# Kernel tuning notes

Measured on AMD Instinct MI355X. Metric: run time of the kernel, lower is better.

The kernel has to match this reference:

```python
import jax, jax.numpy as jnp
import numpy as np
import itertools

D_FEAT = 8      # feature dim per point
N_NBR = 16     # kNN neighbors (self.N)
ORDERS = (2, 3)
BIG = 99999999.0


def _to_select(N, order):
    # rows: [0] + each (order-1)-combination of {1..N-1}, first N-1 rows
    rows = [[0] + list(c) for c in itertools.combinations(range(1, N), order - 1)][:N - 1]
    return np.asarray(rows, dtype=np.int32)  # (N-1, order)


def setup_inputs() -> dict:
    key = jax.random.key(0)
    ks = jax.random.split(key, 18)
    B, NP, DM, DO, NM, PNM = 4, 4096, 16, 8, 64, 64
    r = lambda k, s: jax.random.normal(k, s, dtype=jnp.float32)
    return {
        "x": r(ks[0], (B, NP * D_FEAT)),
        "z": r(ks[1], (B, PNM)),
        "Wm2": r(ks[2], (2, DM)) * 0.5, "bm2": r(ks[3], (DM,)) * 0.1,
        "Wm3": r(ks[4], (3, DM)) * 0.5, "bm3": r(ks[5], (DM,)) * 0.1,
        "Wv2": r(ks[6], (2, DM)) * 0.5, "bv2": r(ks[7], (DM,)) * 0.1,
        "Wv3": r(ks[8], (3, DM)) * 0.5, "bv3": r(ks[9], (DM,)) * 0.1,
        "Wmx": r(ks[10], (2 * DM, DO)) * 0.1, "bmx": r(ks[11], (DO,)) * 0.1,
        "Wvx": r(ks[12], (2 * DM, NM)) * 0.1, "bvx": r(ks[13], (NM,)) * 0.1,
        "Wmz": r(ks[14], (PNM, DO)) * 0.1, "bmz": r(ks[15], (DO,)) * 0.1,
        "Wvz": r(ks[16], (PNM, NM)) * 0.1, "bvz": r(ks[17], (NM,)) * 0.1,
    }


def _forward(x, z, Wm2, bm2, Wm3, bm3, Wv2, bv2, Wv3, bv3,
             Wmx, bmx, Wvx, bvx, Wmz, bmz, Wvz, bvz):
    B = x.shape[0]
    NP = x.shape[1] // D_FEAT
    N = N_NBR
    x3 = x.reshape(B, NP, D_FEAT)

    # pairwise euclidean distances via gram trick (avoids B*NP*NP*D intermediate)
    n2 = jnp.sum(x3 * x3, axis=-1)                                   # (B, NP)
    d2 = n2[:, :, None] + n2[:, None, :] - 2.0 * jnp.einsum('bid,bjd->bij', x3, x3)
    dist = jnp.sqrt(jnp.maximum(d2, 0.0))                            # (B, NP, NP)
    dist = jnp.where(dist == 0.0, BIG, dist)                         # mask exact-zero distances
    diag = jnp.arange(NP)
    dist = dist.at[:, diag, diag].set(BIG)                           # self-distance (exactly 0 in torch)

    # N smallest, sorted ascending
    _, idx = jax.lax.top_k(-dist, N)                                 # idx: (B, NP, N)

    def order_feats(Wf, bf, order):
        ts = jnp.asarray(_to_select(N, order))                       # (N-1, order)
        sel = idx[:, :, ts]                                          # (B, NP, N-1, o)
        g = jax.vmap(lambda xb, sb: xb[sb])(x3, sel)                 # (B, NP, N-1, o, D)
        # Linear(order -> d_Mfeat) applied per feature-dim o-tuple, relu, mean over feature dims
        y = jax.nn.relu(jnp.einsum('bnrod,ok->bnrdk', g, Wf) + bf)   # (B, NP, N-1, D, K)
        return y.mean(axis=3).reshape(B, NP * (N - 1), -1)           # (B, NP*(N-1), K)

    moments = jnp.concatenate([order_feats(Wm2, bm2, 2), order_feats(Wm3, bm3, 3)], axis=-1)
    v_moments = jnp.concatenate([order_feats(Wv2, bv2, 2), order_feats(Wv3, bv3, 3)], axis=-1)

    d_out = Wmx.shape[1]
    x_new = jax.nn.relu(moments @ Wmx + bmx + (z @ Wmz + bmz)[:, None, :])
    x_new = x_new.reshape(B, NP, N - 1, d_out).mean(axis=2).reshape(B, NP * d_out)

    z_new = jax.nn.relu(v_moments @ Wvx + bvx + (z @ Wvz + bvz)[:, None, :]).mean(axis=1)
    return x_new, z_new


def reference(x, z, Wm2, bm2, Wm3, bm3, Wv2, bv2, Wv3, bv3,
              Wmx, bmx, Wvx, bvx, Wmz, bmz, Wvz, bvz):
    return _forward(x, z, Wm2, bm2, Wm3, bm3, Wv2, bv2, Wv3, bv3,
                    Wmx, bmx, Wvx, bvx, Wmz, bmz, Wvz, bvz)
```

## Files before the change

### kernel.cpp

```cpp
#include <hip/hip_runtime.h>
#include <hip/hip_bf16.h>

#define BIGF 99999999.0f
#define NPP 4096
#define BB 4
#define NQ 4


__device__ __forceinline__ float rl(float v, int l) {
    return __int_as_float(__builtin_amdgcn_readlane(__float_as_int(v), l));
}

template <typename T>
__device__ __forceinline__ T bitonic_sort64(T v, int lane) {
    #pragma unroll
    for (int k = 2; k <= 64; k <<= 1) {
        #pragma unroll
        for (int j = k >> 1; j > 0; j >>= 1) {
            T p = __shfl_xor(v, j);
            bool up  = ((lane & k) == 0);
            bool low = ((lane & j) == 0);
            T mn = (v < p) ? v : p;
            T mx = (v < p) ? p : v;
            v = (up == low) ? mn : mx;
        }
    }
    return v;
}

__device__ __forceinline__ unsigned d2key(const float* qf, float n2i,
                                          const float4& a, const float4& c,
                                          float n2j, int j, int q) {
    float dot = 0.f;
    dot = fmaf(qf[0], a.x, dot); dot = fmaf(qf[1], a.y, dot);
    dot = fmaf(qf[2], a.z, dot); dot = fmaf(qf[3], a.w, dot);
    dot = fmaf(qf[4], c.x, dot); dot = fmaf(qf[5], c.y, dot);
    dot = fmaf(qf[6], c.z, dot); dot = fmaf(qf[7], c.w, dot);
    float d2 = fmaf(-2.0f, dot, n2i + n2j);
    return (d2 <= 0.0f || j == q) ? __float_as_uint(BIGF) : __float_as_uint(d2);
}


__global__ __launch_bounds__(256) void n2_kernel(const float* __restrict__ x,
                                                 float* __restrict__ n2tab,
                                                 float* __restrict__ zout) {
    int i = blockIdx.x * 256 + threadIdx.x;
    if (blockIdx.x == 0) zout[threadIdx.x] = 0.f;
    const float4* p = (const float4*)(x + (long)i * 8);
    float4 a = p[0], c = p[1];
    float s = 0.f;
    s = fmaf(a.x, a.x, s); s = fmaf(a.y, a.y, s);
    s = fmaf(a.z, a.z, s); s = fmaf(a.w, a.w, s);
    s = fmaf(c.x, c.x, s); s = fmaf(c.y, c.y, s);
    s = fmaf(c.z, c.z, s); s = fmaf(c.w, c.w, s);
    n2tab[i] = s;
}


__global__ void zz_kernel(const float* __restrict__ z,
                          const float* __restrict__ Wmz, const float* __restrict__ bmz,
                          const float* __restrict__ Wvz, const float* __restrict__ bvz,
                          float* __restrict__ zzm, float* __restrict__ zzv) {
    int b = blockIdx.x, l = threadIdx.x;
    float sv = 0.f;
    for (int p = 0; p < 64; ++p) sv = fmaf(z[b * 64 + p], Wvz[p * 64 + l], sv);
    zzv[b * 64 + l] = sv + bvz[l];
    if (l < 8) {
        float sm = 0.f;
        for (int p = 0; p < 64; ++p) sm = fmaf(z[b * 64 + p], Wmz[p * 8 + l], sm);
        zzm[b * 8 + l] = sm + bmz[l];
    }
}


__global__ __launch_bounds__(256) void knn_kernel(const float* __restrict__ x,
                                                  const float* __restrict__ n2tab,
                                                  int* __restrict__ idx_out) {
    __shared__ unsigned long long cand[4][NQ][64];

    int lane = threadIdx.x & 63;
    int wid  = threadIdx.x >> 6;
    int gw   = blockIdx.x * 4 + wid;
    int q0   = gw * NQ;
    int b    = q0 >> 12;
    int qloc = q0 & 4095;
    const float* xb = x + (long)b * NPP * 8;
    const float* nb = n2tab + b * NPP;

    float qf[NQ][8];
    float n2i[NQ];
    #pragma unroll
    for (int q = 0; q < NQ; ++q) {
        #pragma unroll
        for (int f = 0; f < 8; ++f) qf[q][f] = xb[(qloc + q) * 8 + f];
        n2i[q] = nb[qloc + q];
    }

    unsigned minb[NQ];
    #pragma unroll
    for (int q = 0; q < NQ; ++q) minb[q] = 0xFFFFFFFFu;

    #pragma unroll 4
    for (int t = 0; t < 64; ++t) {
        int j = t * 64 + lane;
        const float4* pj = (const float4*)(xb + j * 8);
        float4 a = pj[0], c = pj[1];
        float n2j = nb[j];
        #pragma unroll
        for (int q = 0; q < NQ; ++q) {
            unsigned kb = d2key(qf[q], n2i[q], a, c, n2j, j, qloc + q);
            minb[q] = (kb < minb[q]) ? kb : minb[q];
        }
    }

    unsigned T[NQ];
    #pragma unroll
    for (int q = 0; q < NQ; ++q) {
        unsigned v = bitonic_sort64(minb[q], lane);
        T[q] = (unsigned)__shfl((int)v, 15);
    }

    int cnt[NQ];
    #pragma unroll
    for (int q = 0; q < NQ; ++q) cnt[q] = 0;

    for (int t = 0; t < 64; ++t) {
        int j = t * 64 + lane;
        const float4* pj = (const float4*)(xb + j * 8);
        float4 a = pj[0], c = pj[1];
        float n2j = nb[j];
        #pragma unroll
        for (int q = 0; q < NQ; ++q) {
            unsigned kb = d2key(qf[q], n2i[q], a, c, n2j, j, qloc + q);
            bool pred = (kb <= T[q]);
            unsigned long long m = __ballot(pred);
            if (m) {
                int ofs = cnt[q] + __popcll(m & ((1ull << lane) - 1ull));
                if (pred && ofs < 64) {
                    cand[wid][q][ofs] = ((unsigned long long)kb << 32) | (unsigned)j;
                }
                cnt[q] += __popcll(m);
            }
        }
    }

    #pragma unroll 1
    for (int q = 0; q < NQ; ++q) {
        int c = cnt[q] < 64 ? cnt[q] : 64;
        unsigned long long key = (lane < c) ? cand[wid][q][lane] : ~0ull;
        key = bitonic_sort64(key, lane);
        if (lane < 16) {
            idx_out[(long)(q0 + q) * 16 + lane] = (int)(key & 0xFFFFFFFFull);
        }
    }
}


__global__ __launch_bounds__(256) void feat_kernel(
    const float* __restrict__ x, const int* __restrict__ idxw,
    const float* __restrict__ Wm2, const float* __restrict__ bm2,
    const float* __restrict__ Wm3, const float* __restrict__ bm3,
    const float* __restrict__ Wv2, const float* __restrict__ bv2,
    const float* __restrict__ Wv3, const float* __restrict__ bv3,
    const float* __restrict__ Wmx, const float* __restrict__ bmx,
    const float* __restrict__ Wvx, const float* __restrict__ bvx,
    const float* __restrict__ zzm, const float* __restrict__ zzv,
    float* __restrict__ xout, float* __restrict__ zout)
{
    int lane = threadIdx.x & 63;
    int wid  = threadIdx.x >> 6;
    int pn   = blockIdx.x * 4 + wid;
    int b    = pn >> 12;
    const float* xb = x + b * NPP * 8;

    __shared__ float xg_s[4][16][8];
    __shared__ float mm_s[4][15][36];
    __shared__ float wmx_s[32][8];
    __shared__ float bzm_s[8];
    __shared__ float zpart[4][64];

    if (threadIdx.x < 256) {
        wmx_s[threadIdx.x >> 3][threadIdx.x & 7] = Wmx[threadIdx.x];
    }
    if (threadIdx.x < 8) bzm_s[threadIdx.x] = bmx[threadIdx.x] + zzm[b * 8 + threadIdx.x];

    int k = lane & 15;
    float w20 = Wm2[k], w21 = Wm2[16 + k], bb2 = bm2[k];
    float w30 = Wm3[k], w31 = Wm3[16 + k], w32 = Wm3[32 + k], bb3 = bm3[k];
    float u20 = Wv2[k], u21 = Wv2[16 + k], cc2 = bv2[k];
    float u30 = Wv3[k], u31 = Wv3[16 + k], u32 = Wv3[32 + k], cc3 = bv3[k];
    float wvx[32];
    #pragma unroll
    for (int c = 0; c < 32; ++c) wvx[c] = Wvx[c * 64 + lane];
    float bz3 = bvx[lane] + zzv[b * 64 + lane];

    if (lane < 16) {
        int myid = idxw[(long)pn * 16 + lane];
        const float4* ps = (const float4*)(xb + (long)myid * 8);
        float4 a = ps[0], c4 = ps[1];
        *((float4*)&xg_s[wid][lane][0]) = a;
        *((float4*)&xg_s[wid][lane][4]) = c4;
    }
    __syncthreads();

    float g0[8];
    #pragma unroll
    for (int f = 0; f < 8; ++f) g0[f] = xg_s[wid][0][f];

    float am2[4], am3[4], av2[4], av3[4];
    #pragma unroll
    for (int p = 0; p < 4; ++p) {
        int rg = lane >> 4;
        int r  = p * 4 + rg;
        int rc = (r < 14) ? r : 14;
        int i2  = rc + 1;
        int i3a = (rc < 14) ? 1 : 2;
        int i3b = (rc < 14) ? rc + 2 : 3;
        const float* G1  = xg_s[wid][i2];
        const float* G3a = xg_s[wid][i3a];
        const float* G3b = xg_s[wid][i3b];
        float s2 = 0.f, s3 = 0.f, t2 = 0.f, t3 = 0.f;
        #pragma unroll
        for (int d = 0; d < 8; ++d) {
            float gz = g0[d], g1 = G1[d], ga = G3a[d], gb = G3b[d];
            float y2 = fmaf(gz, w20, fmaf(g1, w21, bb2));
            s2 += fmaxf(y2, 0.f);
            float y3 = fmaf(gz, w30, fmaf(ga, w31, fmaf(gb, w32, bb3)));
            s3 += fmaxf(y3, 0.f);
            float z2 = fmaf(gz, u20, fmaf(g1, u21, cc2));
            t2 += fmaxf(z2, 0.f);
            float z3 = fmaf(gz, u30, fmaf(ga, u31, fmaf(gb, u32, cc3)));
            t3 += fmaxf(z3, 0.f);
        }
        am2[p] = s2 * 0.125f; am3[p] = s3 * 0.125f;
        av2[p] = t2 * 0.125f; av3[p] = t3 * 0.125f;
        if (r < 15) {
            mm_s[wid][r][k]      = am2[p];
            mm_s[wid][r][16 + k] = am3[p];
        }
    }
    __syncthreads();

    float xa = 0.f;
    #pragma unroll
    for (int half = 0; half < 2; ++half) {
        int r   = (lane >> 3) + half * 8;
        int doo = lane & 7;
        float s = 0.f;
        if (r < 15) {
            s = bzm_s[doo];
            #pragma unroll
            for (int c = 0; c < 32; ++c)
                s = fmaf(mm_s[wid][r][c], wmx_s[c][doo], s);
            s = fmaxf(s, 0.f);
        }
        xa += s;
    }
    xa += __shfl_xor(xa, 8);
    xa += __shfl_xor(xa, 16);
    xa += __shfl_xor(xa, 32);
    float xv = xa * (1.0f / 15.0f);
    if (lane < 8) xout[(long)pn * 8 + lane] = xv;

    float za = 0.f;
    #pragma unroll
    for (int r = 0; r < 15; ++r) {
        float s = bz3;
        const int p  = r >> 2;
        const int sb = (r & 3) * 16;
        #pragma unroll
        for (int c = 0; c < 16; ++c)
            s = fmaf(rl(av2[p], sb + c), wvx[c], s);
        #pragma unroll
        for (int c = 0; c < 16; ++c)
            s = fmaf(rl(av3[p], sb + c), wvx[16 + c], s);
        za += fmaxf(s, 0.f);
    }
    za *= (1.0f / 61440.0f);

    zpart[wid][lane] = za;
    __syncthreads();
    if (wid == 0) {
        float ssum = zpart[0][lane] + zpart[1][lane] + zpart[2][lane] + zpart[3][lane];
        atomicAdd(&zout[b * 64 + lane], ssum);
    }
}


extern "C" void kernel_launch(void* const* d_in, const int* in_sizes, int n_in,
                              void* d_out, int out_size, void* d_ws, size_t ws_size,
                              hipStream_t stream) {
    const float* x   = (const float*)d_in[0];
    const float* z   = (const float*)d_in[1];
    const float* Wm2 = (const float*)d_in[2];
    const float* bm2 = (const float*)d_in[3];
    const float* Wm3 = (const float*)d_in[4];
    const float* bm3 = (const float*)d_in[5];
    const float* Wv2 = (const float*)d_in[6];
    const float* bv2 = (const float*)d_in[7];
    const float* Wv3 = (const float*)d_in[8];
    const float* bv3 = (const float*)d_in[9];
    const float* Wmx = (const float*)d_in[10];
    const float* bmx = (const float*)d_in[11];
    const float* Wvx = (const float*)d_in[12];
    const float* bvx = (const float*)d_in[13];
    const float* Wmz = (const float*)d_in[14];
    const float* bmz = (const float*)d_in[15];
    const float* Wvz = (const float*)d_in[16];
    const float* bvz = (const float*)d_in[17];

    float* out  = (float*)d_out;
    int*   idxw = (int*)d_ws;
    float* zzm  = (float*)((char*)d_ws + (size_t)BB * NPP * 16 * 4);
    float* zzv  = zzm + BB * 8;
    float* n2t  = zzv + BB * 64;
    float* xout = out;
    float* zout = out + BB * NPP * 8;

    n2_kernel<<<dim3(BB * NPP / 256), dim3(256), 0, stream>>>(x, n2t, zout);
    zz_kernel<<<dim3(BB), dim3(64), 0, stream>>>(z, Wmz, bmz, Wvz, bvz, zzm, zzv);
    knn_kernel<<<dim3(BB * NPP / (4 * NQ)), dim3(256), 0, stream>>>(x, n2t, idxw);
    feat_kernel<<<dim3(4096), dim3(256), 0, stream>>>(
        x, idxw, Wm2, bm2, Wm3, bm3, Wv2, bv2, Wv3, bv3,
        Wmx, bmx, Wvx, bvx, zzm, zzv, xout, zout);
}
```

Before: 266.7 us.

## Rework kNN candidate collection, fuse z-projection into n2 kernel, stage moments in LDS

```diff
diff --git a/kernel.cpp b/kernel.cpp
--- a/kernel.cpp
+++ b/kernel.cpp
@@ -5,11 +5,8 @@
 #define NPP 4096
 #define BB 4
 #define NQ 4
-
-
-__device__ __forceinline__ float rl(float v, int l) {
-    return __int_as_float(__builtin_amdgcn_readlane(__float_as_int(v), l));
-}
+#define CAP 128
+
 
 template <typename T>
 __device__ __forceinline__ T bitonic_sort64(T v, int lane) {
@@ -28,24 +25,15 @@
     return v;
 }
 
-__device__ __forceinline__ unsigned d2key(const float* qf, float n2i,
-                                          const float4& a, const float4& c,
-                                          float n2j, int j, int q) {
-    float dot = 0.f;
-    dot = fmaf(qf[0], a.x, dot); dot = fmaf(qf[1], a.y, dot);
-    dot = fmaf(qf[2], a.z, dot); dot = fmaf(qf[3], a.w, dot);
-    dot = fmaf(qf[4], c.x, dot); dot = fmaf(qf[5], c.y, dot);
-    dot = fmaf(qf[6], c.z, dot); dot = fmaf(qf[7], c.w, dot);
-    float d2 = fmaf(-2.0f, dot, n2i + n2j);
-    return (d2 <= 0.0f || j == q) ? __float_as_uint(BIGF) : __float_as_uint(d2);
-}
-
-
-__global__ __launch_bounds__(256) void n2_kernel(const float* __restrict__ x,
-                                                 float* __restrict__ n2tab,
-                                                 float* __restrict__ zout) {
+
+__global__ __launch_bounds__(256) void n2_kernel(
+    const float* __restrict__ x, const float* __restrict__ z,
+    const float* __restrict__ Wmz, const float* __restrict__ bmz,
+    const float* __restrict__ Wvz, const float* __restrict__ bvz,
+    float* __restrict__ n2tab, float* __restrict__ zzm, float* __restrict__ zzv,
+    float* __restrict__ zout)
+{
     int i = blockIdx.x * 256 + threadIdx.x;
-    if (blockIdx.x == 0) zout[threadIdx.x] = 0.f;
     const float4* p = (const float4*)(x + (long)i * 8);
     float4 a = p[0], c = p[1];
     float s = 0.f;
@@ -54,21 +42,19 @@
     s = fmaf(c.x, c.x, s); s = fmaf(c.y, c.y, s);
     s = fmaf(c.z, c.z, s); s = fmaf(c.w, c.w, s);
     n2tab[i] = s;
-}
-
-
-__global__ void zz_kernel(const float* __restrict__ z,
-                          const float* __restrict__ Wmz, const float* __restrict__ bmz,
-                          const float* __restrict__ Wvz, const float* __restrict__ bvz,
-                          float* __restrict__ zzm, float* __restrict__ zzv) {
-    int b = blockIdx.x, l = threadIdx.x;
-    float sv = 0.f;
-    for (int p = 0; p < 64; ++p) sv = fmaf(z[b * 64 + p], Wvz[p * 64 + l], sv);
-    zzv[b * 64 + l] = sv + bvz[l];
-    if (l < 8) {
-        float sm = 0.f;
-        for (int p = 0; p < 64; ++p) sm = fmaf(z[b * 64 + p], Wmz[p * 8 + l], sm);
-        zzm[b * 8 + l] = sm + bmz[l];
+
+    if (blockIdx.x == 0) {
+        zout[threadIdx.x] = 0.f;
+        int b = threadIdx.x >> 6, l = threadIdx.x & 63;
+        float sv = 0.f;
+        for (int q = 0; q < 64; ++q) sv = fmaf(z[b * 64 + q], Wvz[q * 64 + l], sv);
+        zzv[b * 64 + l] = sv + bvz[l];
+        if (threadIdx.x < 32) {
+            int bm = threadIdx.x >> 3, lm = threadIdx.x & 7;
+            float sm = 0.f;
+            for (int q = 0; q < 64; ++q) sm = fmaf(z[bm * 64 + q], Wmz[q * 8 + lm], sm);
+            zzm[bm * 8 + lm] = sm + bmz[lm];
+        }
     }
 }
 
@@ -76,10 +62,13 @@
 __global__ __launch_bounds__(256) void knn_kernel(const float* __restrict__ x,
                                                   const float* __restrict__ n2tab,
                                                   int* __restrict__ idx_out) {
-    __shared__ unsigned long long cand[4][NQ][64];
+    __shared__ unsigned long long cand[4][NQ][CAP];
+    __shared__ unsigned cnt_s[4][NQ];
 
     int lane = threadIdx.x & 63;
     int wid  = threadIdx.x >> 6;
+    if (lane < NQ) cnt_s[wid][lane] = 0;
+
     int gw   = blockIdx.x * 4 + wid;
     int q0   = gw * NQ;
     int b    = q0 >> 12;
@@ -89,68 +78,103 @@
 
     float qf[NQ][8];
     float n2i[NQ];
+    int selfT[NQ], selfL[NQ];
     #pragma unroll
     for (int q = 0; q < NQ; ++q) {
         #pragma unroll
         for (int f = 0; f < 8; ++f) qf[q][f] = xb[(qloc + q) * 8 + f];
-        n2i[q] = nb[qloc + q];
-    }
-
-    unsigned minb[NQ];
-    #pragma unroll
-    for (int q = 0; q < NQ; ++q) minb[q] = 0xFFFFFFFFu;
-
-    #pragma unroll 4
+        n2i[q]   = nb[qloc + q];
+        selfT[q] = (qloc + q) >> 6;
+        selfL[q] = (qloc + q) & 63;
+    }
+    const unsigned BIGB = __float_as_uint(BIGF);
+
+    unsigned long long mn[NQ];
+    #pragma unroll
+    for (int q = 0; q < NQ; ++q) mn[q] = ~0ull;
+
+    #pragma unroll 2
     for (int t = 0; t < 64; ++t) {
         int j = t * 64 + lane;
-        const float4* pj = (const float4*)(xb + j * 8);
+        const float4* pj = (const float4*)(xb + (long)j * 8);
         float4 a = pj[0], c = pj[1];
         float n2j = nb[j];
         #pragma unroll
         for (int q = 0; q < NQ; ++q) {
-            unsigned kb = d2key(qf[q], n2i[q], a, c, n2j, j, qloc + q);
-            minb[q] = (kb < minb[q]) ? kb : minb[q];
+            float dot = 0.f;
+            dot = fmaf(qf[q][0], a.x, dot); dot = fmaf(qf[q][1], a.y, dot);
+            dot = fmaf(qf[q][2], a.z, dot); dot = fmaf(qf[q][3], a.w, dot);
+            dot = fmaf(qf[q][4], c.x, dot); dot = fmaf(qf[q][5], c.y, dot);
+            dot = fmaf(qf[q][6], c.z, dot); dot = fmaf(qf[q][7], c.w, dot);
+            float d2 = fmaf(-2.0f, dot, n2i[q] + n2j);
+            unsigned kb = (d2 <= 0.0f) ? BIGB : __float_as_uint(d2);
+            if (t == selfT[q]) {
+                kb = (lane == selfL[q]) ? BIGB : kb;
+            }
+            unsigned long long key = ((unsigned long long)kb << 32) | (unsigned)j;
+            mn[q] = (key < mn[q]) ? key : mn[q];
         }
     }
 
     unsigned T[NQ];
     #pragma unroll
     for (int q = 0; q < NQ; ++q) {
-        unsigned v = bitonic_sort64(minb[q], lane);
-        T[q] = (unsigned)__shfl((int)v, 15);
-    }
-
-    int cnt[NQ];
-    #pragma unroll
-    for (int q = 0; q < NQ; ++q) cnt[q] = 0;
-
+        unsigned long long s = bitonic_sort64(mn[q], lane);
+        T[q] = (unsigned)(__shfl(s, 15) >> 32);
+    }
+
+    #pragma unroll 2
     for (int t = 0; t < 64; ++t) {
         int j = t * 64 + lane;
-        const float4* pj = (const float4*)(xb + j * 8);
+        const float4* pj = (const float4*)(xb + (long)j * 8);
         float4 a = pj[0], c = pj[1];
         float n2j = nb[j];
+        unsigned kb[NQ];
+        bool hit = false;
         #pragma unroll
         for (int q = 0; q < NQ; ++q) {
-            unsigned kb = d2key(qf[q], n2i[q], a, c, n2j, j, qloc + q);
-            bool pred = (kb <= T[q]);
-            unsigned long long m = __ballot(pred);
-            if (m) {
-                int ofs = cnt[q] + __popcll(m & ((1ull << lane) - 1ull));
-                if (pred && ofs < 64) {
-                    cand[wid][q][ofs] = ((unsigned long long)kb << 32) | (unsigned)j;
+            float dot = 0.f;
+            dot = fmaf(qf[q][0], a.x, dot); dot = fmaf(qf[q][1], a.y, dot);
+            dot = fmaf(qf[q][2], a.z, dot); dot = fmaf(qf[q][3], a.w, dot);
+            dot = fmaf(qf[q][4], c.x, dot); dot = fmaf(qf[q][5], c.y, dot);
+            dot = fmaf(qf[q][6], c.z, dot); dot = fmaf(qf[q][7], c.w, dot);
+            float d2 = fmaf(-2.0f, dot, n2i[q] + n2j);
+            unsigned k = (d2 <= 0.0f) ? BIGB : __float_as_uint(d2);
+            if (t == selfT[q]) {
+                k = (lane == selfL[q]) ? BIGB : k;
+            }
+            kb[q] = k;
+            hit |= (k <= T[q]);
+        }
+        if (__any(hit)) {
+            #pragma unroll
+            for (int q = 0; q < NQ; ++q) {
+                if (kb[q] <= T[q]) {
+                    unsigned old = atomicAdd(&cnt_s[wid][q], 1u);
+                    if (old < CAP) {
+                        cand[wid][q][old] =
+                            ((unsigned long long)kb[q] << 32) | (unsigned)j;
+                    }
                 }
-                cnt[q] += __popcll(m);
             }
         }
     }
 
     #pragma unroll 1
     for (int q = 0; q < NQ; ++q) {
-        int c = cnt[q] < 64 ? cnt[q] : 64;
-        unsigned long long key = (lane < c) ? cand[wid][q][lane] : ~0ull;
-        key = bitonic_sort64(key, lane);
+        unsigned nc = cnt_s[wid][q];
+        int n = nc > CAP ? CAP : (int)nc;
+        unsigned long long v = (lane < n) ? cand[wid][q][lane] : ~0ull;
+        unsigned long long R = bitonic_sort64(v, lane);
+        if (n > 64) {
+            unsigned long long w2 = (64 + lane < n) ? cand[wid][q][64 + lane] : ~0ull;
+            w2 = bitonic_sort64(w2, lane);
+            unsigned long long vt = __shfl(w2, lane - 16);
+            unsigned long long comb = (lane < 16) ? R : ((lane < 32) ? vt : ~0ull);
+            R = bitonic_sort64(comb, lane);
+        }
         if (lane < 16) {
-            idx_out[(long)(q0 + q) * 16 + lane] = (int)(key & 0xFFFFFFFFull);
+            idx_out[(long)(q0 + q) * 16 + lane] = (int)(R & 0xFFFFFFFFull);
         }
     }
 }
@@ -174,7 +198,7 @@
     const float* xb = x + b * NPP * 8;
 
     __shared__ float xg_s[4][16][8];
-    __shared__ float mm_s[4][15][36];
+    __shared__ float mo_s[4][15][68];
     __shared__ float wmx_s[32][8];
     __shared__ float bzm_s[8];
     __shared__ float zpart[4][64];
@@ -207,7 +231,6 @@
     #pragma unroll
     for (int f = 0; f < 8; ++f) g0[f] = xg_s[wid][0][f];
 
-    float am2[4], am3[4], av2[4], av3[4];
     #pragma unroll
     for (int p = 0; p < 4; ++p) {
         int rg = lane >> 4;
@@ -232,11 +255,11 @@
             float z3 = fmaf(gz, u30, fmaf(ga, u31, fmaf(gb, u32, cc3)));
             t3 += fmaxf(z3, 0.f);
         }
-        am2[p] = s2 * 0.125f; am3[p] = s3 * 0.125f;
-        av2[p] = t2 * 0.125f; av3[p] = t3 * 0.125f;
         if (r < 15) {
-            mm_s[wid][r][k]      = am2[p];
-            mm_s[wid][r][16 + k] = am3[p];
+            mo_s[wid][r][k]      = s2 * 0.125f;
+            mo_s[wid][r][16 + k] = s3 * 0.125f;
+            mo_s[wid][r][32 + k] = t2 * 0.125f;
+            mo_s[wid][r][48 + k] = t3 * 0.125f;
         }
     }
     __syncthreads();
@@ -250,8 +273,13 @@
         if (r < 15) {
             s = bzm_s[doo];
             #pragma unroll
-            for (int c = 0; c < 32; ++c)
-                s = fmaf(mm_s[wid][r][c], wmx_s[c][doo], s);
+            for (int cc = 0; cc < 8; ++cc) {
+                float4 v = *(const float4*)&mo_s[wid][r][cc * 4];
+                s = fmaf(v.x, wmx_s[cc * 4 + 0][doo], s);
+                s = fmaf(v.y, wmx_s[cc * 4 + 1][doo], s);
+                s = fmaf(v.z, wmx_s[cc * 4 + 2][doo], s);
+                s = fmaf(v.w, wmx_s[cc * 4 + 3][doo], s);
+            }
             s = fmaxf(s, 0.f);
         }
         xa += s;
@@ -263,17 +291,18 @@
     if (lane < 8) xout[(long)pn * 8 + lane] = xv;
 
     float za = 0.f;
-    #pragma unroll
+    #pragma unroll 1
     for (int r = 0; r < 15; ++r) {
+        const float* row = &mo_s[wid][r][32];
         float s = bz3;
-        const int p  = r >> 2;
-        const int sb = (r & 3) * 16;
-        #pragma unroll
-        for (int c = 0; c < 16; ++c)
-            s = fmaf(rl(av2[p], sb + c), wvx[c], s);
-        #pragma unroll
-        for (int c = 0; c < 16; ++c)
-            s = fmaf(rl(av3[p], sb + c), wvx[16 + c], s);
+        #pragma unroll
+        for (int cc = 0; cc < 8; ++cc) {
+            float4 v = *(const float4*)(row + cc * 4);
+            s = fmaf(v.x, wvx[cc * 4 + 0], s);
+            s = fmaf(v.y, wvx[cc * 4 + 1], s);
+            s = fmaf(v.z, wvx[cc * 4 + 2], s);
+            s = fmaf(v.w, wvx[cc * 4 + 3], s);
+        }
         za += fmaxf(s, 0.f);
     }
     za *= (1.0f / 61440.0f);
@@ -317,8 +346,8 @@
     float* xout = out;
     float* zout = out + BB * NPP * 8;
 
-    n2_kernel<<<dim3(BB * NPP / 256), dim3(256), 0, stream>>>(x, n2t, zout);
-    zz_kernel<<<dim3(BB), dim3(64), 0, stream>>>(z, Wmz, bmz, Wvz, bvz, zzm, zzv);
+    n2_kernel<<<dim3(BB * NPP / 256), dim3(256), 0, stream>>>(
+        x, z, Wmz, bmz, Wvz, bvz, n2t, zzm, zzv, zout);
     knn_kernel<<<dim3(BB * NPP / (4 * NQ)), dim3(256), 0, stream>>>(x, n2t, idxw);
     feat_kernel<<<dim3(4096), dim3(256), 0, stream>>>(
         x, idxw, Wm2, bm2, Wm3, bm3, Wv2, bv2, Wv3, bv3,
```

Result: faster. 243.4 us (-8.7%).
